# Kernel tuning notes

Hardware: AMD Instinct MI355X
Metric: run time of the kernel (lower is better)

Reference implementation:

```python
import jax, jax.numpy as jnp
import numpy as np

WINDOW = 11  # sliding window width (odd)


def setup_inputs() -> dict:
    key = jax.random.key(0)
    k1, k2, k3 = jax.random.split(key, 3)
    LENGTH, RANK = 200000, 64
    time_factor = jax.random.normal(k1, (LENGTH, RANK), dtype=jnp.float32)
    # nn.Linear(RANK, RANK): weight (out,in), bias (out,)
    W = jax.random.normal(k2, (RANK, RANK), dtype=jnp.float32) / np.sqrt(RANK)
    b = jax.random.normal(k3, (RANK,), dtype=jnp.float32) * 0.01
    return {"time_factor": time_factor, "W": W, "b": b}


def reference(time_factor, W, b):
    row, col = time_factor.shape
    pad = (WINDOW - 1) // 2
    # F.pad on transposed data pads the row (time) dimension with zeros
    padded = jnp.pad(time_factor, ((pad, pad), (0, 0)))
    # indexer: blocks[i] = padded[i : i+WINDOW]  -> (row, WINDOW, col)
    idx = jnp.arange(row)[:, None] + jnp.arange(WINDOW)[None, :]
    blocks = padded[idx]
    # var1 = tanh(Linear(data))  (exp contains '_tanh')
    var1 = jnp.tanh(time_factor @ W.T + b)            # (row, col)
    # var2 = bmm(blocks, var1) -> per-row window scores
    var2 = jnp.einsum('rwc,rc->rw', blocks, var1)      # (row, WINDOW)
    # exp ends with 'scaled'
    var2 = var2 / jnp.sqrt(jnp.asarray(col, time_factor.dtype))
    # exp starts with 'softmax' (softmax over window dim)
    var2 = jax.nn.softmax(var2, axis=1)
    # var3 = bmm(scores, blocks) -> smoothed factor
    out = jnp.einsum('rw,rwc->rc', var2, blocks)       # (row, col)
    return out
```

## Files before the change

### kernel.cpp

```cpp
#include <hip/hip_runtime.h>
#include <hip/hip_bf16.h>


constexpr int RANK   = 64;
constexpr int WINDOW = 11;
constexpr int PAD    = 5;
constexpr int TILE   = 16;
constexpr int BLOCK  = 256;
constexpr int TR     = 64;
constexpr int BSTR   = 68;
constexpr int GRIDB  = 768;

typedef short short8  __attribute__((ext_vector_type(8)));
typedef float float4v __attribute__((ext_vector_type(4)));

constexpr int V1_S = 72;
constexpr int SC_S = 18;

__device__ __forceinline__ short8 cvt_bf8(float4 a, float4 b) {
    union { short8 s; __hip_bfloat162 h[4]; } u;
    u.h[0] = __float22bfloat162_rn(make_float2(a.x, a.y));
    u.h[1] = __float22bfloat162_rn(make_float2(a.z, a.w));
    u.h[2] = __float22bfloat162_rn(make_float2(b.x, b.y));
    u.h[3] = __float22bfloat162_rn(make_float2(b.z, b.w));
    return u.s;
}

__device__ __forceinline__ float fast_tanh(float x) {
    return 1.0f - 2.0f / (1.0f + __expf(2.0f * x));
}

__global__ __launch_bounds__(BLOCK, 3) void attn_win_kernel(
    const float* __restrict__ A,
    const float* __restrict__ W,
    const float* __restrict__ b,
    float* __restrict__ out,
    int rows)
{
    __shared__ __align__(16) float          band[4][32][BSTR];
    __shared__ __align__(16) __hip_bfloat16 V1[4][TILE][V1_S];
    __shared__ __align__(16) float          Sc[4][32][SC_S];

    const int lane = threadIdx.x & 63;
    const int wv   = threadIdx.x >> 6;
    const int m16  = lane & 15;
    const int quad = lane >> 4;
    const int sr   = lane >> 4;
    const int sc4  = (lane & 15) * 4;

    short8 wfrag[4][2];
    #pragma unroll
    for (int ct = 0; ct < 4; ct++) {
        #pragma unroll
        for (int kf = 0; kf < 2; kf++) {
            const float4* p =
                (const float4*)(W + (ct * 16 + m16) * RANK + kf * 32 + quad * 8);
            wfrag[ct][kf] = cvt_bf8(p[0], p[1]);
        }
    }
    float bias[4];
    #pragma unroll
    for (int ct = 0; ct < 4; ct++) bias[ct] = b[ct * 16 + m16];

    const int n_btiles = (rows + TR - 1) / TR;
    int bt = blockIdx.x;
    if (bt >= n_btiles) return;

    {
        const int rw0 = bt * TR + wv * TILE;
        float4 stg[8];
        #pragma unroll
        for (int j = 0; j < 8; j++) {
            const int g = rw0 - PAD + j * 4 + sr;
            stg[j] = ((unsigned)g < (unsigned)rows)
                         ? *(const float4*)(A + (size_t)g * RANK + sc4)
                         : make_float4(0.f, 0.f, 0.f, 0.f);
        }
        #pragma unroll
        for (int j = 0; j < 8; j++)
            *(float4*)&band[wv][j * 4 + sr][sc4] = stg[j];
    }

    for (; bt < n_btiles; bt += gridDim.x) {
        const int rw = bt * TR + wv * TILE;

        short8 abnd[2][2];
        short8 am1[2];
        #pragma unroll
        for (int it = 0; it < 2; it++)
            #pragma unroll
            for (int kf = 0; kf < 2; kf++) {
                const float4* pp =
                    (const float4*)&band[wv][it * 16 + m16][kf * 32 + quad * 8];
                abnd[it][kf] = cvt_bf8(pp[0], pp[1]);
            }
        #pragma unroll
        for (int kf = 0; kf < 2; kf++) {
            const float4* pp =
                (const float4*)&band[wv][PAD + m16][kf * 32 + quad * 8];
            am1[kf] = cvt_bf8(pp[0], pp[1]);
        }

        float4 stg[8];
        {
            const int rwn = (bt + (int)gridDim.x) * TR + wv * TILE;
            #pragma unroll
            for (int j = 0; j < 8; j++) {
                const int g = rwn - PAD + j * 4 + sr;
                stg[j] = ((unsigned)g < (unsigned)rows)
                             ? *(const float4*)(A + (size_t)g * RANK + sc4)
                             : make_float4(0.f, 0.f, 0.f, 0.f);
            }
        }

        float4v acc[4];
        #pragma unroll
        for (int ct = 0; ct < 4; ct++)
            acc[ct] = (float4v){bias[ct], bias[ct], bias[ct], bias[ct]};
        #pragma unroll
        for (int kf = 0; kf < 2; kf++)
            #pragma unroll
            for (int ct = 0; ct < 4; ct++)
                acc[ct] = __builtin_amdgcn_mfma_f32_16x16x32_bf16(
                    am1[kf], wfrag[ct][kf], acc[ct], 0, 0, 0);
        #pragma unroll
        for (int ct = 0; ct < 4; ct++)
            #pragma unroll
            for (int rg = 0; rg < 4; rg++)
                V1[wv][quad * 4 + rg][ct * 16 + m16] =
                    __float2bfloat16(fast_tanh(acc[ct][rg]));

        float4v sacc[2];
        sacc[0] = (float4v){0.f, 0.f, 0.f, 0.f};
        sacc[1] = (float4v){0.f, 0.f, 0.f, 0.f};
        #pragma unroll
        for (int kf = 0; kf < 2; kf++) {
            const short8 bfr =
                *(const short8*)&V1[wv][m16][kf * 32 + quad * 8];
            #pragma unroll
            for (int it = 0; it < 2; it++)
                sacc[it] = __builtin_amdgcn_mfma_f32_16x16x32_bf16(
                    abnd[it][kf], bfr, sacc[it], 0, 0, 0);
        }
        #pragma unroll
        for (int it = 0; it < 2; it++)
            #pragma unroll
            for (int rg = 0; rg < 4; rg++)
                Sc[wv][it * 16 + quad * 4 + rg][m16] = sacc[it][rg];

        float p[WINDOW];
        {
            float s[WINDOW];
            float mx = -1e30f;
            #pragma unroll
            for (int w = 0; w < WINDOW; w++) {
                s[w] = Sc[wv][m16 + w][m16];
                mx = fmaxf(mx, s[w]);
            }
            float den = 0.0f;
            #pragma unroll
            for (int w = 0; w < WINDOW; w++) {
                p[w] = __expf((s[w] - mx) * 0.125f);
                den += p[w];
            }
            const float rden = __fdividef(1.0f, den);
            #pragma unroll
            for (int w = 0; w < WINDOW; w++) p[w] *= rden;
        }

        float aw[26];
        #pragma unroll
        for (int s = 0; s < 26; s++) aw[s] = band[wv][s][lane];

        #pragma unroll
        for (int j = 0; j < 8; j++)
            *(float4*)&band[wv][j * 4 + sr][sc4] = stg[j];

        #pragma unroll
        for (int rr = 0; rr < TILE; rr++) {
            float o = 0.0f;
            #pragma unroll
            for (int w = 0; w < WINDOW; w++) {
                const float pw = __uint_as_float(
                    __builtin_amdgcn_readlane(__float_as_uint(p[w]), rr));
                o = fmaf(pw, aw[rr + w], o);
            }
            if (rw + rr < rows)
                out[(size_t)(rw + rr) * RANK + lane] = o;
        }
    }
}

extern "C" void kernel_launch(void* const* d_in, const int* in_sizes, int n_in,
                              void* d_out, int out_size, void* d_ws, size_t ws_size,
                              hipStream_t stream) {
    const float* A = (const float*)d_in[0];
    const float* W = (const float*)d_in[1];
    const float* b = (const float*)d_in[2];
    float* out = (float*)d_out;

    const int rows     = in_sizes[0] / RANK;
    const int n_btiles = (rows + TR - 1) / TR;
    const int blocks   = n_btiles < GRIDB ? n_btiles : GRIDB;

    hipLaunchKernelGGL(attn_win_kernel, dim3(blocks), dim3(BLOCK), 0, stream,
                       A, W, b, out, rows);
}
```

Measured before the change: 117.2 us.

## Replace V1 LDS round-trip with transposed MFMA and ds_bpermute, shrink band

Computes the Linear layer as a transposed MFMA (W times A) so the tanh outputs can be packed to bf16 in registers and redistributed with ds_bpermute, removing the V1 shared-memory buffer and its store/load. The band buffer shrinks from 32 to 28 rows with 7 staging loads instead of 8, and the next-tile prefetch is moved later to lower register pressure. Shared memory is merged into one array, occupancy is set to 4 waves per EU, and the grid grows to 1024 blocks. The cost is extra bpermute cross-lane traffic and a tighter register budget under the occupancy target.

Measured after the change: 120.4 us. 2.8% more time.

```diff
diff --git a/kernel.cpp b/kernel.cpp
--- a/kernel.cpp
+++ b/kernel.cpp
@@ -8,14 +8,17 @@
 constexpr int TILE   = 16;
 constexpr int BLOCK  = 256;
 constexpr int TR     = 64;
+constexpr int BROWS  = 28;
 constexpr int BSTR   = 68;
-constexpr int GRIDB  = 768;
+constexpr int SC_S   = 18;
+constexpr int GRIDB  = 1024;
+
+constexpr int BAND_F = BROWS * BSTR;
+constexpr int SC_OFF = 4 * BAND_F;
+constexpr int SMEMF  = SC_OFF + 4 * 32 * SC_S;
 
 typedef short short8  __attribute__((ext_vector_type(8)));
 typedef float float4v __attribute__((ext_vector_type(4)));
-
-constexpr int V1_S = 72;
-constexpr int SC_S = 18;
 
 __device__ __forceinline__ short8 cvt_bf8(float4 a, float4 b) {
     union { short8 s; __hip_bfloat162 h[4]; } u;
@@ -30,16 +33,16 @@
     return 1.0f - 2.0f / (1.0f + __expf(2.0f * x));
 }
 
-__global__ __launch_bounds__(BLOCK, 3) void attn_win_kernel(
+__global__ __launch_bounds__(BLOCK)
+__attribute__((amdgpu_waves_per_eu(4, 4)))
+void attn_win_kernel(
     const float* __restrict__ A,
     const float* __restrict__ W,
     const float* __restrict__ b,
     float* __restrict__ out,
     int rows)
 {
-    __shared__ __align__(16) float          band[4][32][BSTR];
-    __shared__ __align__(16) __hip_bfloat16 V1[4][TILE][V1_S];
-    __shared__ __align__(16) float          Sc[4][32][SC_S];
+    __shared__ __align__(16) float smem[SMEMF];
 
     const int lane = threadIdx.x & 63;
     const int wv   = threadIdx.x >> 6;
@@ -48,6 +51,9 @@
     const int sr   = lane >> 4;
     const int sc4  = (lane & 15) * 4;
 
+    float* const bandW = smem + wv * BAND_F;
+    float* const ScW   = smem + SC_OFF + wv * 32 * SC_S;
+
     short8 wfrag[4][2];
     #pragma unroll
     for (int ct = 0; ct < 4; ct++) {
@@ -58,9 +64,13 @@
             wfrag[ct][kf] = cvt_bf8(p[0], p[1]);
         }
     }
-    float bias[4];
+    float4 biasT[4];
     #pragma unroll
-    for (int ct = 0; ct < 4; ct++) bias[ct] = b[ct * 16 + m16];
+    for (int ct = 0; ct < 4; ct++)
+        biasT[ct] = *(const float4*)(b + ct * 16 + quad * 4);
+
+    const int idxA = 4 * m16 + 128 * (quad & 1);
+    const int idxB = idxA + 64;
 
     const int n_btiles = (rows + TR - 1) / TR;
     int bt = blockIdx.x;
@@ -68,85 +78,102 @@
 
     {
         const int rw0 = bt * TR + wv * TILE;
-        float4 stg[8];
-        #pragma unroll
-        for (int j = 0; j < 8; j++) {
-            const int g = rw0 - PAD + j * 4 + sr;
-            stg[j] = ((unsigned)g < (unsigned)rows)
-                         ? *(const float4*)(A + (size_t)g * RANK + sc4)
-                         : make_float4(0.f, 0.f, 0.f, 0.f);
-        }
-        #pragma unroll
-        for (int j = 0; j < 8; j++)
-            *(float4*)&band[wv][j * 4 + sr][sc4] = stg[j];
+        #pragma unroll
+        for (int ro = 0; ro < 7; ro++) {
+            const int g = rw0 - PAD + ro * 4 + sr;
+            float4 x = make_float4(0.f, 0.f, 0.f, 0.f);
+            if ((unsigned)g < (unsigned)rows)
+                x = *(const float4*)(A + (size_t)g * RANK + sc4);
+            *(float4*)&bandW[(ro * 4 + sr) * BSTR + sc4] = x;
+        }
     }
 
     for (; bt < n_btiles; bt += gridDim.x) {
         const int rw = bt * TR + wv * TILE;
 
-        short8 abnd[2][2];
         short8 am1[2];
-        #pragma unroll
-        for (int it = 0; it < 2; it++)
-            #pragma unroll
-            for (int kf = 0; kf < 2; kf++) {
-                const float4* pp =
-                    (const float4*)&band[wv][it * 16 + m16][kf * 32 + quad * 8];
-                abnd[it][kf] = cvt_bf8(pp[0], pp[1]);
-            }
         #pragma unroll
         for (int kf = 0; kf < 2; kf++) {
             const float4* pp =
-                (const float4*)&band[wv][PAD + m16][kf * 32 + quad * 8];
+                (const float4*)&bandW[(PAD + m16) * BSTR + kf * 32 + quad * 8];
             am1[kf] = cvt_bf8(pp[0], pp[1]);
         }
 
-        float4 stg[8];
-        {
-            const int rwn = (bt + (int)gridDim.x) * TR + wv * TILE;
-            #pragma unroll
-            for (int j = 0; j < 8; j++) {
-                const int g = rwn - PAD + j * 4 + sr;
-                stg[j] = ((unsigned)g < (unsigned)rows)
-                             ? *(const float4*)(A + (size_t)g * RANK + sc4)
-                             : make_float4(0.f, 0.f, 0.f, 0.f);
-            }
-        }
-
-        float4v acc[4];
+        float4v accT[4];
         #pragma unroll
         for (int ct = 0; ct < 4; ct++)
-            acc[ct] = (float4v){bias[ct], bias[ct], bias[ct], bias[ct]};
+            accT[ct] = (float4v){biasT[ct].x, biasT[ct].y,
+                                 biasT[ct].z, biasT[ct].w};
         #pragma unroll
         for (int kf = 0; kf < 2; kf++)
             #pragma unroll
             for (int ct = 0; ct < 4; ct++)
-                acc[ct] = __builtin_amdgcn_mfma_f32_16x16x32_bf16(
-                    am1[kf], wfrag[ct][kf], acc[ct], 0, 0, 0);
+                accT[ct] = __builtin_amdgcn_mfma_f32_16x16x32_bf16(
+                    wfrag[ct][kf], am1[kf], accT[ct], 0, 0, 0);
+
+        int pk[4][2];
         #pragma unroll
         for (int ct = 0; ct < 4; ct++)
             #pragma unroll
-            for (int rg = 0; rg < 4; rg++)
-                V1[wv][quad * 4 + rg][ct * 16 + m16] =
-                    __float2bfloat16(fast_tanh(acc[ct][rg]));
+            for (int u = 0; u < 2; u++) {
+                union { __hip_bfloat162 h; int i; } cv;
+                cv.h = __float22bfloat162_rn(make_float2(
+                    fast_tanh(accT[ct][2 * u]),
+                    fast_tanh(accT[ct][2 * u + 1])));
+                pk[ct][u] = cv.i;
+            }
+
+        short8 bfr[2];
+        #pragma unroll
+        for (int kf = 0; kf < 2; kf++) {
+            union { int w[4]; short8 s; } u;
+            #pragma unroll
+            for (int w = 0; w < 4; w++) {
+                const int idx = (w >> 1) ? idxB : idxA;
+                const int lo = __builtin_amdgcn_ds_bpermute(idx, pk[2 * kf][w & 1]);
+                const int hi = __builtin_amdgcn_ds_bpermute(idx, pk[2 * kf + 1][w & 1]);
+                u.w[w] = (quad >= 2) ? hi : lo;
+            }
+            bfr[kf] = u.s;
+        }
+
+        short8 abnd[2][2];
+        #pragma unroll
+        for (int it = 0; it < 2; it++)
+            #pragma unroll
+            for (int kf = 0; kf < 2; kf++) {
+                const float4* pp = (const float4*)
+                    &bandW[(it * 16 + m16) * BSTR + kf * 32 + quad * 8];
+                abnd[it][kf] = cvt_bf8(pp[0], pp[1]);
+            }
 
         float4v sacc[2];
         sacc[0] = (float4v){0.f, 0.f, 0.f, 0.f};
         sacc[1] = (float4v){0.f, 0.f, 0.f, 0.f};
         #pragma unroll
-        for (int kf = 0; kf < 2; kf++) {
-            const short8 bfr =
-                *(const short8*)&V1[wv][m16][kf * 32 + quad * 8];
+        for (int kf = 0; kf < 2; kf++)
             #pragma unroll
             for (int it = 0; it < 2; it++)
                 sacc[it] = __builtin_amdgcn_mfma_f32_16x16x32_bf16(
-                    abnd[it][kf], bfr, sacc[it], 0, 0, 0);
-        }
+                    abnd[it][kf], bfr[kf], sacc[it], 0, 0, 0);
+
         #pragma unroll
         for (int it = 0; it < 2; it++)
             #pragma unroll
             for (int rg = 0; rg < 4; rg++)
-                Sc[wv][it * 16 + quad * 4 + rg][m16] = sacc[it][rg];
+                ScW[(it * 16 + quad * 4 + rg) * SC_S + m16] = sacc[it][rg];
+
+        float4 stg[7];
+        {
+            const int rwn = rw + (int)gridDim.x * TR;
+            #pragma unroll
+            for (int ro = 0; ro < 7; ro++) {
+                const int g = rwn - PAD + ro * 4 + sr;
+                stg[ro] = make_float4(0.f, 0.f, 0.f, 0.f);
+                if ((unsigned)g < (unsigned)rows)
+                    stg[ro] = *(const float4*)(A + (size_t)g * RANK + sc4);
+            }
+        }
 
         float p[WINDOW];
         {
@@ -154,7 +181,7 @@
             float mx = -1e30f;
             #pragma unroll
             for (int w = 0; w < WINDOW; w++) {
-                s[w] = Sc[wv][m16 + w][m16];
+                s[w] = ScW[(m16 + w) * SC_S + m16];
                 mx = fmaxf(mx, s[w]);
             }
             float den = 0.0f;
@@ -170,11 +197,11 @@
 
         float aw[26];
         #pragma unroll
-        for (int s = 0; s < 26; s++) aw[s] = band[wv][s][lane];
-
-        #pragma unroll
-        for (int j = 0; j < 8; j++)
-            *(float4*)&band[wv][j * 4 + sr][sc4] = stg[j];
+        for (int s = 0; s < 26; s++) aw[s] = bandW[s * BSTR + lane];
+
+        #pragma unroll
+        for (int ro = 0; ro < 7; ro++)
+            *(float4*)&bandW[(ro * 4 + sr) * BSTR + sc4] = stg[ro];
 
         #pragma unroll
         for (int rr = 0; rr < TILE; rr++) {
```
